# Kernel optimization log

Measured on AMD Instinct MI355X. Metric: run time of the kernel, lower is better.

The kernel has to match this reference:

```python
import jax, jax.numpy as jnp
from jax import lax
import numpy as np

VOCAB, EMBED, HIDDEN, BATCH, MAXLEN = 32000, 512, 1024, 64, 64


def setup_inputs() -> dict:
    key = jax.random.key(0)
    ks = jax.random.split(key, 18)
    s = 0.02
    H, E, V = HIDDEN, EMBED, VOCAB
    return {
        "thought": jax.random.normal(ks[0], (BATCH, H), jnp.float32),
        "emb_table": jax.random.normal(ks[1], (V, E), jnp.float32) * s,
        "w_ih0": jax.random.normal(ks[2], (4 * H, E + H), jnp.float32) * s,
        "w_hh0": jax.random.normal(ks[3], (4 * H, H), jnp.float32) * s,
        "b_ih0": jax.random.normal(ks[4], (4 * H,), jnp.float32) * s,
        "b_hh0": jax.random.normal(ks[5], (4 * H,), jnp.float32) * s,
        "w_ih1": jax.random.normal(ks[6], (4 * H, H), jnp.float32) * s,
        "w_hh1": jax.random.normal(ks[7], (4 * H, H), jnp.float32) * s,
        "b_ih1": jax.random.normal(ks[8], (4 * H,), jnp.float32) * s,
        "b_hh1": jax.random.normal(ks[9], (4 * H,), jnp.float32) * s,
        "gw1": jax.random.normal(ks[10], (H, H), jnp.float32) * s,
        "gb1": jax.random.normal(ks[11], (H,), jnp.float32) * s,
        "gw2": jax.random.normal(ks[12], (1, H), jnp.float32) * s,
        "gb2": jax.random.normal(ks[13], (1,), jnp.float32) * s,
        "out_w": jax.random.normal(ks[14], (V, H), jnp.float32) * s,
        "out_b": jax.random.normal(ks[15], (V,), jnp.float32) * s,
        "max_len": MAXLEN,
    }


def lstm_cell(x, h, c, w_ih, w_hh, b_ih, b_hh):
    # torch nn.LSTM gate order: i, f, g, o
    g = x @ w_ih.T + b_ih + h @ w_hh.T + b_hh
    i, f, gg, o = jnp.split(g, 4, axis=-1)
    c2 = jax.nn.sigmoid(f) * c + jax.nn.sigmoid(i) * jnp.tanh(gg)
    return jax.nn.sigmoid(o) * jnp.tanh(c2), c2


def reference(thought, emb_table, w_ih0, w_hh0, b_ih0, b_hh0, w_ih1, w_hh1,
              b_ih1, b_hh1, gw1, gb1, gw2, gb2, out_w, out_b, max_len):
    """Generation branch of BioDecoder.forward (captions=None), eval mode, epoch=0."""
    B, H = thought.shape
    V = out_w.shape[0]
    temperature, top_p, top_k = 0.9, 0.88, 60
    key = jax.random.key(42)
    rows = jnp.arange(B)[:, None]

    def filt(logits):
        # top-k filter
        kth = lax.top_k(logits, top_k)[0][:, -1:]
        logits = jnp.where(logits < kth, -jnp.inf, logits)
        # nucleus (top-p) filter
        sl, si = lax.top_k(logits, V)  # full descending sort
        cum = jnp.cumsum(jax.nn.softmax(sl, axis=-1), axis=-1)
        rm = cum > top_p
        rm = jnp.concatenate([jnp.zeros_like(rm[:, :1]), rm[:, :-1]], axis=-1)  # always keep best
        mask = jnp.zeros_like(rm).at[rows, si].set(rm)
        return jnp.where(mask, -jnp.inf, logits)

    def step(carry, t):
        h1, c1, h2, c2, prev_ctx, word, counts, hist = carry
        x = jnp.concatenate([emb_table[word], prev_ctx], axis=-1)  # [B, E+H]
        h1, c1 = lstm_cell(x, h1, c1, w_ih0, w_hh0, b_ih0, b_hh0)
        h2, c2 = lstm_cell(h1, h2, c2, w_ih1, w_hh1, b_ih1, b_hh1)
        gate = jax.nn.sigmoid(jnp.tanh(h2 @ gw1.T + gb1) @ gw2.T + gb2)  # [B,1]
        out = h2 * gate
        logits = out @ out_w.T + out_b  # [B, V]
        # recency-decayed repetition penalty over full generated history
        ar = jnp.arange(hist.shape[0])
        w = jnp.where(ar < t, 2.5 * jnp.power(0.8, jnp.maximum(t - ar, 0).astype(jnp.float32)), 0.0)
        pen = jnp.zeros((B, V), logits.dtype).at[rows, hist.T].add(
            jnp.broadcast_to(w[None, :], (B, hist.shape[0])))
        # global count penalty (token_counts shared across batch, as in source)
        logits = logits - pen - jnp.where(counts > 1, 2.0 * counts, 0.0)[None, :]
        logits = logits / temperature + (0.3 / (counts + 1.0))[None, :]
        logits = filt(logits)
        nxt = jax.random.categorical(jax.random.fold_in(key, t), logits, axis=-1)  # [B]
        counts = counts.at[nxt].add(1.0)
        hist = hist.at[t].set(nxt)
        return (h1, c1, h2, c2, out, nxt, counts, hist), nxt

    zeros_h = jnp.zeros_like(thought)
    carry0 = (thought, zeros_h, thought, zeros_h, thought,
              jnp.full((B,), 1, jnp.int32),
              jnp.zeros((V,), jnp.float32),
              jnp.zeros((max_len, B), jnp.int32))
    _, tokens = lax.scan(step, carry0, jnp.arange(max_len))
    return tokens.T  # [B, max_len]
```

## Files before the change

### kernel.cpp

```cpp
#include <hip/hip_runtime.h>
#include <stdint.h>
#include <math.h>

#pragma clang fp contract(off)

#define BATCH 64
#define HID   1024
#define EMBD  512
#define VOC   32000
#define MAXT  64
#define NTOPK 60
#define CAND_MAX 256

__device__ __forceinline__ float xla_tanh(float x) {
  float ax = fabsf(x);
  float xc = fminf(fmaxf(x, -9.0f), 9.0f);
  float x2 = xc * xc;
  float num = -2.76076847742355e-16f;
  num = fmaf(x2, num, 2.00018790482477e-13f);
  num = fmaf(x2, num, -8.60467152213735e-11f);
  num = fmaf(x2, num, 5.12229709037114e-08f);
  num = fmaf(x2, num, 1.48572235717979e-05f);
  num = fmaf(x2, num, 6.37261928875436e-04f);
  num = fmaf(x2, num, 4.89352455891786e-03f);
  num = xc * num;
  float den = 1.19825839466702e-06f;
  den = fmaf(x2, den, 1.18534705686654e-04f);
  den = fmaf(x2, den, 2.26843463243900e-03f);
  den = fmaf(x2, den, 4.89352518554385e-03f);
  float r = num / den;
  return (ax < 0.0004f) ? x : r;
}

__device__ __forceinline__ float xla_sigmoid(float x) {
  return 0.5f * xla_tanh(0.5f * x) + 0.5f;
}

__device__ __forceinline__ float cephes_expf(float _x) {
  float x = fminf(_x, 88.723164f);
  x = fmaxf(x, -88.723164f);
  float m = floorf(fmaf(x, 1.44269504088896341f, 0.5f));
  float r = fmaf(m, -0.693359375f, x);
  r = fmaf(m, 2.12194440e-4f, r);
  float r2 = r * r;
  float r3 = r2 * r;
  float y, y1, y2;
  y  = fmaf(1.9875691500E-4f, r, 1.3981999507E-3f);
  y1 = fmaf(4.1665795894E-2f, r, 1.6666665459E-1f);
  y2 = r + 1.0f;
  y  = fmaf(y, r, 8.3334519073E-3f);
  y1 = fmaf(y1, r, 5.0000001201E-1f);
  y  = fmaf(y, r3, y1);
  y  = fmaf(y, r2, y2);
  float res = ldexpf(y, (int)m);
  return fmaxf(res, _x);
}

__device__ __forceinline__ float cephes_logf(float _x) {
  float x = fmaxf(_x, 1.17549435e-38f);
  unsigned ux = __float_as_uint(x);
  int e_int = (int)(ux >> 23) - 126;
  x = __uint_as_float((ux & 0x007FFFFFu) | 0x3F000000u);
  float e = (float)e_int;
  if (x < 0.707106781186547524f) { e -= 1.0f; x = x + x - 1.0f; }
  else { x = x - 1.0f; }
  float z = x * x;
  float y = 7.0376836292E-2f;
  y = fmaf(y, x, -1.1514610310E-1f);
  y = fmaf(y, x,  1.1676998740E-1f);
  y = fmaf(y, x, -1.2420140846E-1f);
  y = fmaf(y, x,  1.4249322787E-1f);
  y = fmaf(y, x, -1.6668057665E-1f);
  y = fmaf(y, x,  2.0000714765E-1f);
  y = fmaf(y, x, -2.4999993993E-1f);
  y = fmaf(y, x,  3.3333331174E-1f);
  y = y * x;
  y = y * z;
  y = fmaf(e, -2.12194440e-4f, y);
  y = fmaf(-0.5f, z, y);
  float r = x + y;
  r = fmaf(e, 0.693359375f, r);
  return r;
}

__device__ __forceinline__ unsigned rotl32(unsigned v, int s) {
  return (v << s) | (v >> (32 - s));
}
__device__ __forceinline__ void threefry(unsigned k0, unsigned k1,
                                         unsigned& x0, unsigned& x1) {
  unsigned k2 = k0 ^ k1 ^ 0x1BD11BDAu;
  x0 += k0; x1 += k1;
  x0 += x1; x1 = rotl32(x1, 13); x1 ^= x0;
  x0 += x1; x1 = rotl32(x1, 15); x1 ^= x0;
  x0 += x1; x1 = rotl32(x1, 26); x1 ^= x0;
  x0 += x1; x1 = rotl32(x1,  6); x1 ^= x0;
  x0 += k1; x1 += k2 + 1u;
  x0 += x1; x1 = rotl32(x1, 17); x1 ^= x0;
  x0 += x1; x1 = rotl32(x1, 29); x1 ^= x0;
  x0 += x1; x1 = rotl32(x1, 16); x1 ^= x0;
  x0 += x1; x1 = rotl32(x1, 24); x1 ^= x0;
  x0 += k2; x1 += k0 + 2u;
  x0 += x1; x1 = rotl32(x1, 13); x1 ^= x0;
  x0 += x1; x1 = rotl32(x1, 15); x1 ^= x0;
  x0 += x1; x1 = rotl32(x1, 26); x1 ^= x0;
  x0 += x1; x1 = rotl32(x1,  6); x1 ^= x0;
  x0 += k0; x1 += k1 + 3u;
  x0 += x1; x1 = rotl32(x1, 17); x1 ^= x0;
  x0 += x1; x1 = rotl32(x1, 29); x1 ^= x0;
  x0 += x1; x1 = rotl32(x1, 16); x1 ^= x0;
  x0 += x1; x1 = rotl32(x1, 24); x1 ^= x0;
  x0 += k1; x1 += k2 + 4u;
  x0 += x1; x1 = rotl32(x1, 13); x1 ^= x0;
  x0 += x1; x1 = rotl32(x1, 15); x1 ^= x0;
  x0 += x1; x1 = rotl32(x1, 26); x1 ^= x0;
  x0 += x1; x1 = rotl32(x1,  6); x1 ^= x0;
  x0 += k2; x1 += k0 + 5u;
}

__device__ __forceinline__ float gumbel_val(unsigned k0, unsigned k1, int b, int v) {
  unsigned x0 = 0u, x1 = (unsigned)(b * VOC + v);
  threefry(k0, k1, x0, x1);
  unsigned bits = x0 ^ x1;
  float u = __uint_as_float(0x3f800000u | (bits >> 9)) - 1.0f;
  if (u == 0.0f) u = 1.17549435e-38f;
  return -cephes_logf(-cephes_logf(u));
}

__device__ __forceinline__ unsigned okey(float f) {
  unsigned u = __float_as_uint(f);
  return (u & 0x80000000u) ? ~u : (u | 0x80000000u);
}
__device__ __forceinline__ float okey_inv(unsigned key) {
  unsigned u = (key & 0x80000000u) ? (key & 0x7FFFFFFFu) : ~key;
  return __uint_as_float(u);
}

__global__ __launch_bounds__(256) void k_init(const float* __restrict__ thought,
    float* h1a, float* h2a, float* c1, float* c2, float* prev_ctx,
    float* counts, int* word, int* hist) {
  int i = blockIdx.x * blockDim.x + threadIdx.x;
  if (i < BATCH * HID) {
    float tv = thought[i];
    h1a[i] = tv; h2a[i] = tv; prev_ctx[i] = tv;
    c1[i] = 0.f; c2[i] = 0.f;
  }
  if (i < VOC) counts[i] = 0.f;
  if (i < BATCH) word[i] = 1;
  if (i < MAXT * BATCH) hist[i] = 0;
}

__global__ __launch_bounds__(256) void k_gates0f(const float* __restrict__ emb,
    const int* __restrict__ word, const float* __restrict__ prev_ctx,
    const float* __restrict__ h1r, const float* __restrict__ w_ih,
    const float* __restrict__ b_ih, const float* __restrict__ w_hh,
    const float* __restrict__ b_hh, float* __restrict__ h1w,
    float* __restrict__ c1) {
  int jl = threadIdx.x & 7, bg = threadIdx.x >> 3;
  int gate = jl & 3, usel = jl >> 2;
  int u = blockIdx.x * 2 + usel;
  int j = gate * 1024 + u;
  __shared__ float sg[2][4][64];
  const float4* wi4 = (const float4*)(w_ih + (size_t)j * (EMBD + HID));
  const float4* wh4 = (const float4*)(w_hh + (size_t)j * HID);
  const float4* e4[2]; const float4* p4[2]; const float4* h4[2];
  #pragma unroll
  for (int i = 0; i < 2; ++i) {
    int b = bg + 32 * i;
    e4[i] = (const float4*)(emb + (size_t)word[b] * EMBD);
    p4[i] = (const float4*)(prev_ctx + (size_t)b * HID);
    h4[i] = (const float4*)(h1r + (size_t)b * HID);
  }
  float acc[2] = {0.f, 0.f};
  float shh[2] = {0.f, 0.f};
  for (int k = 0; k < EMBD / 4; ++k) {
    float4 w = wi4[k];
    #pragma unroll
    for (int i = 0; i < 2; ++i) {
      float4 a = e4[i][k];
      acc[i] = fmaf(a.x, w.x, acc[i]); acc[i] = fmaf(a.y, w.y, acc[i]);
      acc[i] = fmaf(a.z, w.z, acc[i]); acc[i] = fmaf(a.w, w.w, acc[i]);
    }
  }
  for (int k = 0; k < HID / 4; ++k) {
    float4 w = wi4[EMBD / 4 + k];
    #pragma unroll
    for (int i = 0; i < 2; ++i) {
      float4 a = p4[i][k];
      acc[i] = fmaf(a.x, w.x, acc[i]); acc[i] = fmaf(a.y, w.y, acc[i]);
      acc[i] = fmaf(a.z, w.z, acc[i]); acc[i] = fmaf(a.w, w.w, acc[i]);
    }
  }
  for (int k = 0; k < HID / 4; ++k) {
    float4 w = wh4[k];
    #pragma unroll
    for (int i = 0; i < 2; ++i) {
      float4 a = h4[i][k];
      shh[i] = fmaf(a.x, w.x, shh[i]); shh[i] = fmaf(a.y, w.y, shh[i]);
      shh[i] = fmaf(a.z, w.z, shh[i]); shh[i] = fmaf(a.w, w.w, shh[i]);
    }
  }
  float bi = b_ih[j], bh = b_hh[j];
  #pragma unroll
  for (int i = 0; i < 2; ++i) {
    int b = bg + 32 * i;
    sg[usel][gate][b] = ((acc[i] + bi) + shh[i]) + bh;
  }
  __syncthreads();
  if (threadIdx.x < 128) {
    int us = threadIdx.x >> 6, b = threadIdx.x & 63;
    int uu = blockIdx.x * 2 + us;
    float iv = sg[us][0][b], fv = sg[us][1][b], gv = sg[us][2][b], ov = sg[us][3][b];
    size_t idx = (size_t)b * HID + uu;
    float cold = c1[idx];
    float cnew = xla_sigmoid(fv) * cold + xla_sigmoid(iv) * xla_tanh(gv);
    c1[idx] = cnew;
    h1w[idx] = xla_sigmoid(ov) * xla_tanh(cnew);
  }
}

__global__ __launch_bounds__(256) void k_gates1f(const float* __restrict__ xin,
    const float* __restrict__ hin, const float* __restrict__ w_ih,
    const float* __restrict__ b_ih, const float* __restrict__ w_hh,
    const float* __restrict__ b_hh, float* __restrict__ h2w,
    float* __restrict__ c2) {
  int jl = threadIdx.x & 7, bg = threadIdx.x >> 3;
  int gate = jl & 3, usel = jl >> 2;
  int u = blockIdx.x * 2 + usel;
  int j = gate * 1024 + u;
  __shared__ float sg[2][4][64];
  const float4* wi4 = (const float4*)(w_ih + (size_t)j * HID);
  const float4* wh4 = (const float4*)(w_hh + (size_t)j * HID);
  float acc[2] = {0.f, 0.f};
  float shh[2] = {0.f, 0.f};
  for (int k = 0; k < HID / 4; ++k) {
    float4 w = wi4[k];
    #pragma unroll
    for (int i = 0; i < 2; ++i) {
      float4 a = ((const float4*)(xin + (size_t)(bg + 32 * i) * HID))[k];
      acc[i] = fmaf(a.x, w.x, acc[i]); acc[i] = fmaf(a.y, w.y, acc[i]);
      acc[i] = fmaf(a.z, w.z, acc[i]); acc[i] = fmaf(a.w, w.w, acc[i]);
    }
  }
  for (int k = 0; k < HID / 4; ++k) {
    float4 w = wh4[k];
    #pragma unroll
    for (int i = 0; i < 2; ++i) {
      float4 a = ((const float4*)(hin + (size_t)(bg + 32 * i) * HID))[k];
      shh[i] = fmaf(a.x, w.x, shh[i]); shh[i] = fmaf(a.y, w.y, shh[i]);
      shh[i] = fmaf(a.z, w.z, shh[i]); shh[i] = fmaf(a.w, w.w, shh[i]);
    }
  }
  float bi = b_ih[j], bh = b_hh[j];
  #pragma unroll
  for (int i = 0; i < 2; ++i) {
    int b = bg + 32 * i;
    sg[usel][gate][b] = ((acc[i] + bi) + shh[i]) + bh;
  }
  __syncthreads();
  if (threadIdx.x < 128) {
    int us = threadIdx.x >> 6, b = threadIdx.x & 63;
    int uu = blockIdx.x * 2 + us;
    float iv = sg[us][0][b], fv = sg[us][1][b], gv = sg[us][2][b], ov = sg[us][3][b];
    size_t idx = (size_t)b * HID + uu;
    float cold = c2[idx];
    float cnew = xla_sigmoid(fv) * cold + xla_sigmoid(iv) * xla_tanh(gv);
    c2[idx] = cnew;
    h2w[idx] = xla_sigmoid(ov) * xla_tanh(cnew);
  }
}

__global__ __launch_bounds__(256) void k_gtmp(const float* __restrict__ h2,
    const float* __restrict__ gw1, const float* __restrict__ gb1,
    float* __restrict__ gtmp) {
  int ul = threadIdx.x & 3, b = threadIdx.x >> 2;
  int u = blockIdx.x * 4 + ul;
  const float4* w4 = (const float4*)(gw1 + (size_t)u * HID);
  const float4* a4 = (const float4*)(h2 + (size_t)b * HID);
  float acc = 0.f;
  for (int k = 0; k < HID / 4; ++k) {
    float4 w = w4[k];
    float4 a = a4[k];
    acc = fmaf(a.x, w.x, acc); acc = fmaf(a.y, w.y, acc);
    acc = fmaf(a.z, w.z, acc); acc = fmaf(a.w, w.w, acc);
  }
  gtmp[(size_t)b * HID + u] = xla_tanh(acc + gb1[u]);
}

__global__ __launch_bounds__(256) void k_gateout(const float* __restrict__ gtmp,
    const float* __restrict__ gw2, const float* __restrict__ gb2,
    const float* __restrict__ h2, float* __restrict__ prev_ctx) {
  int b = blockIdx.x, tid = threadIdx.x;
  __shared__ float red[256];
  __shared__ float gsh;
  float s = 0.f;
  for (int k = tid; k < HID; k += 256)
    s = fmaf(gtmp[(size_t)b * HID + k], gw2[k], s);
  red[tid] = s;
  __syncthreads();
  for (int st = 128; st > 0; st >>= 1) {
    if (tid < st) red[tid] += red[tid + st];
    __syncthreads();
  }
  if (tid == 0) gsh = xla_sigmoid(red[0] + gb2[0]);
  __syncthreads();
  float gate = gsh;
  for (int k = tid; k < HID; k += 256)
    prev_ctx[(size_t)b * HID + k] = h2[(size_t)b * HID + k] * gate;
}

__global__ __launch_bounds__(256) void k_logits(const float* __restrict__ outp,
    const float* __restrict__ out_w, const float* __restrict__ out_b,
    const float* __restrict__ counts, float* __restrict__ raw,
    float* __restrict__ adj) {
  int vl = threadIdx.x & 63;
  int v = blockIdx.x * 64 + vl;
  int bbase = __builtin_amdgcn_readfirstlane((int)(threadIdx.x >> 6) * 16);
  const float4* w4 = (const float4*)(out_w + (size_t)v * HID);
  const float4* ob4 = (const float4*)(outp + (size_t)bbase * HID);
  float acc[16];
  #pragma unroll
  for (int i = 0; i < 16; ++i) acc[i] = 0.f;
  for (int k = 0; k < HID / 4; ++k) {
    float4 w = w4[k];
    #pragma unroll
    for (int i = 0; i < 16; ++i) {
      float4 a = ob4[k + 256 * i];
      acc[i] = fmaf(a.x, w.x, acc[i]); acc[i] = fmaf(a.y, w.y, acc[i]);
      acc[i] = fmaf(a.z, w.z, acc[i]); acc[i] = fmaf(a.w, w.w, acc[i]);
    }
  }
  float c = counts[v];
  float cpen = (c > 1.0f) ? (2.0f * c) : 0.0f;
  float bonus = 0.3f / (c + 1.0f);
  float bv = out_b[v];
  #pragma unroll
  for (int i = 0; i < 16; ++i) {
    int b = bbase + i;
    float r = acc[i] + bv;
    raw[(size_t)b * VOC + v] = r;
    adj[(size_t)b * VOC + v] = (r - cpen) / 0.9f + bonus;
  }
}

__global__ __launch_bounds__(256) void k_sample(float* __restrict__ adj,
    const float* __restrict__ raw, float* __restrict__ counts,
    int* __restrict__ word, int* __restrict__ hist,
    int* __restrict__ out_tokens, int t) {
  int b = blockIdx.x, tid = threadIdx.x;
  float* row = adj + (size_t)b * VOC;
  __shared__ unsigned keys[VOC];
  __shared__ int wcnt[4];
  __shared__ int sh_cnt;
  __shared__ float cval[CAND_MAX];
  __shared__ int cidx[CAND_MAX];
  __shared__ float sval[CAND_MAX];
  __shared__ int sidx[CAND_MAX];
  __shared__ unsigned char kept[CAND_MAX];
  __shared__ float rval[256];
  __shared__ int ridx[256];
  __shared__ unsigned shk0, shk1;
  __shared__ int hcol[MAXT];
  __shared__ float wtab[MAXT];

  if (tid < t) hcol[tid] = hist[tid * BATCH + b];
  if (tid < MAXT) wtab[tid] = 2.5f * powf(0.8f, (float)tid);
  if (tid == 0) {
    sh_cnt = 0;
    unsigned a = 0u, cc = (unsigned)t;
    threefry(0u, 42u, a, cc);
    shk0 = a; shk1 = cc;
  }
  __syncthreads();

  if (tid < t) {
    int ar = tid;
    int tok = hcol[ar];
    bool first = true;
    for (int a2 = 0; a2 < ar; ++a2)
      if (hcol[a2] == tok) { first = false; break; }
    if (first) {
      float pen = 0.f;
      for (int a2 = ar; a2 < t; ++a2)
        if (hcol[a2] == tok) pen += wtab[t - a2];
      float c = counts[tok];
      float cpen = (c > 1.0f) ? (2.0f * c) : 0.0f;
      float bonus = 0.3f / (c + 1.0f);
      float r = raw[(size_t)b * VOC + tok];
      row[tok] = ((r - pen) - cpen) / 0.9f + bonus;
    }
  }
  __syncthreads();

  const float4* row4 = (const float4*)row;
  uint4* keys4 = (uint4*)keys;
  for (int i = tid; i < VOC / 4; i += 256) {
    float4 f = row4[i];
    uint4 kk;
    kk.x = okey(f.x); kk.y = okey(f.y); kk.z = okey(f.z); kk.w = okey(f.w);
    keys4[i] = kk;
  }
  __syncthreads();

  unsigned long long lo = 0ULL, hi = 1ULL << 32;
  for (int it = 0; it < 32; ++it) {
    unsigned mid = (unsigned)((lo + hi) >> 1);
    int cnt = 0;
    for (int i = tid; i < VOC / 4; i += 256) {
      uint4 kk = keys4[i];
      cnt += (kk.x >= mid) ? 1 : 0;
      cnt += (kk.y >= mid) ? 1 : 0;
      cnt += (kk.z >= mid) ? 1 : 0;
      cnt += (kk.w >= mid) ? 1 : 0;
    }
    #pragma unroll
    for (int off = 32; off > 0; off >>= 1)
      cnt += __shfl_xor(cnt, off, 64);
    if ((tid & 63) == 0) wcnt[tid >> 6] = cnt;
    __syncthreads();
    int total = wcnt[0] + wcnt[1] + wcnt[2] + wcnt[3];
    if (total >= NTOPK) lo = (unsigned long long)mid;
    else                hi = (unsigned long long)mid;
    __syncthreads();
  }
  unsigned kmin = (unsigned)lo;

  for (int v = tid; v < VOC; v += 256) {
    unsigned key = keys[v];
    if (key >= kmin) {
      int pos = atomicAdd(&sh_cnt, 1);
      if (pos < CAND_MAX) { cval[pos] = okey_inv(key); cidx[pos] = v; }
    }
  }
  __syncthreads();
  int C = sh_cnt; if (C > CAND_MAX) C = CAND_MAX;

  for (int i = tid; i < C; i += 256) {
    float vi = cval[i]; int ii = cidx[i]; int r = 0;
    for (int j = 0; j < C; ++j) {
      float vj = cval[j]; int ij = cidx[j];
      if (vj > vi || (vj == vi && ij < ii)) ++r;
    }
    sval[r] = vi; sidx[r] = ii;
  }
  __syncthreads();

  if (tid == 0) {
    float m = sval[0];
    float psum = 0.f;
    for (int j = 0; j < C; ++j) {
      float p = cephes_expf(sval[j] - m);
      cval[j] = p;
      psum += p;
    }
    float cum = 0.f;
    for (int j = 0; j < C; ++j) {
      kept[j] = (j == 0 || cum <= 0.88f) ? 1 : 0;
      cum += cval[j] / psum;
    }
  }
  __syncthreads();

  float bscore = -INFINITY; int bidx = 0x7FFFFFFF;
  for (int j = tid; j < C; j += 256) {
    if (kept[j]) {
      float gv = gumbel_val(shk0, shk1, b, sidx[j]);
      float sc = gv + sval[j];
      if (sc > bscore || (sc == bscore && sidx[j] < bidx)) { bscore = sc; bidx = sidx[j]; }
    }
  }
  rval[tid] = bscore; ridx[tid] = bidx;
  __syncthreads();
  for (int s = 128; s > 0; s >>= 1) {
    if (tid < s) {
      float ov = rval[tid + s]; int oi = ridx[tid + s];
      if (ov > rval[tid] || (ov == rval[tid] && oi < ridx[tid])) {
        rval[tid] = ov; ridx[tid] = oi;
      }
    }
    __syncthreads();
  }
  if (tid == 0) {
    int tok = ridx[0];
    word[b] = tok;
    hist[t * BATCH + b] = tok;
    out_tokens[b * MAXT + t] = tok;
    atomicAdd(&counts[tok], 1.0f);
  }
}

extern "C" void kernel_launch(void* const* d_in, const int* in_sizes, int n_in,
                              void* d_out, int out_size, void* d_ws, size_t ws_size,
                              hipStream_t stream) {
  const float* thought = (const float*)d_in[0];
  const float* emb     = (const float*)d_in[1];
  const float* w_ih0   = (const float*)d_in[2];
  const float* w_hh0   = (const float*)d_in[3];
  const float* b_ih0   = (const float*)d_in[4];
  const float* b_hh0   = (const float*)d_in[5];
  const float* w_ih1   = (const float*)d_in[6];
  const float* w_hh1   = (const float*)d_in[7];
  const float* b_ih1   = (const float*)d_in[8];
  const float* b_hh1   = (const float*)d_in[9];
  const float* gw1     = (const float*)d_in[10];
  const float* gb1     = (const float*)d_in[11];
  const float* gw2     = (const float*)d_in[12];
  const float* gb2     = (const float*)d_in[13];
  const float* out_w   = (const float*)d_in[14];
  const float* out_b   = (const float*)d_in[15];
  int* out_tokens = (int*)d_out;

  float* F = (float*)d_ws;
  float* h1a      = F;
  float* h1b      = F + 65536;
  float* h2a      = F + 131072;
  float* h2b      = F + 196608;
  float* c1       = F + 262144;
  float* c2       = F + 327680;
  float* prev_ctx = F + 393216;
  float* gtmp     = F + 458752;
  float* counts   = F + 524288;
  float* raw      = F + 556288;
  float* adj      = F + 2604288;
  int*   word     = (int*)(F + 4652288);
  int*   hist     = word + 64;

  k_init<<<256, 256, 0, stream>>>(thought, h1a, h2a, c1, c2, prev_ctx, counts, word, hist);
  for (int t = 0; t < MAXT; ++t) {
    const float* h1r = (t & 1) ? h1b : h1a;
    float*       h1w = (t & 1) ? h1a : h1b;
    const float* h2r = (t & 1) ? h2b : h2a;
    float*       h2w = (t & 1) ? h2a : h2b;
    k_gates0f<<<512, 256, 0, stream>>>(emb, word, prev_ctx, h1r, w_ih0, b_ih0, w_hh0, b_hh0, h1w, c1);
    k_gates1f<<<512, 256, 0, stream>>>(h1w, h2r, w_ih1, b_ih1, w_hh1, b_hh1, h2w, c2);
    k_gtmp<<<256, 256, 0, stream>>>(h2w, gw1, gb1, gtmp);
    k_gateout<<<64, 256, 0, stream>>>(gtmp, gw2, gb2, h2w, prev_ctx);
    k_logits<<<500, 256, 0, stream>>>(prev_ctx, out_w, out_b, counts, raw, adj);
    k_sample<<<64, 256, 0, stream>>>(adj, raw, counts, word, hist, out_tokens, t);
  }
}
```

Before: 39.32 ms.

## Fuse per-step LSTM decode kernels into one persistent kernel with grid barriers

Replaces the six kernel launches per time step (LSTM layer 0, layer 1, gate MLP, gate output, logits, sampling) and the init kernel with one persistent kernel of 224 blocks. The phases are separated by a software grid barrier built on an atomic counter. This removes hundreds of launches and their gaps, and drops the gtmp scratch buffer. Each block now handles four hidden units per LSTM iteration instead of two. The cost is that the large shared-memory key array limits each CU to one resident block, so occupancy in the memory-bound matvecs drops. The kernel also relies on all 224 blocks being co-resident, otherwise the spinning barrier deadlocks.

```diff
diff --git a/kernel.cpp b/kernel.cpp
--- a/kernel.cpp
+++ b/kernel.cpp
@@ -11,6 +11,7 @@
 #define MAXT  64
 #define NTOPK 60
 #define CAND_MAX 256
+#define NB    224
 
 __device__ __forceinline__ float xla_tanh(float x) {
   float ax = fabsf(x);
@@ -135,221 +136,35 @@
   return __uint_as_float(u);
 }
 
-__global__ __launch_bounds__(256) void k_init(const float* __restrict__ thought,
-    float* h1a, float* h2a, float* c1, float* c2, float* prev_ctx,
-    float* counts, int* word, int* hist) {
-  int i = blockIdx.x * blockDim.x + threadIdx.x;
-  if (i < BATCH * HID) {
-    float tv = thought[i];
-    h1a[i] = tv; h2a[i] = tv; prev_ctx[i] = tv;
-    c1[i] = 0.f; c2[i] = 0.f;
-  }
-  if (i < VOC) counts[i] = 0.f;
-  if (i < BATCH) word[i] = 1;
-  if (i < MAXT * BATCH) hist[i] = 0;
-}
-
-__global__ __launch_bounds__(256) void k_gates0f(const float* __restrict__ emb,
-    const int* __restrict__ word, const float* __restrict__ prev_ctx,
-    const float* __restrict__ h1r, const float* __restrict__ w_ih,
-    const float* __restrict__ b_ih, const float* __restrict__ w_hh,
-    const float* __restrict__ b_hh, float* __restrict__ h1w,
-    float* __restrict__ c1) {
-  int jl = threadIdx.x & 7, bg = threadIdx.x >> 3;
-  int gate = jl & 3, usel = jl >> 2;
-  int u = blockIdx.x * 2 + usel;
-  int j = gate * 1024 + u;
-  __shared__ float sg[2][4][64];
-  const float4* wi4 = (const float4*)(w_ih + (size_t)j * (EMBD + HID));
-  const float4* wh4 = (const float4*)(w_hh + (size_t)j * HID);
-  const float4* e4[2]; const float4* p4[2]; const float4* h4[2];
-  #pragma unroll
-  for (int i = 0; i < 2; ++i) {
-    int b = bg + 32 * i;
-    e4[i] = (const float4*)(emb + (size_t)word[b] * EMBD);
-    p4[i] = (const float4*)(prev_ctx + (size_t)b * HID);
-    h4[i] = (const float4*)(h1r + (size_t)b * HID);
-  }
-  float acc[2] = {0.f, 0.f};
-  float shh[2] = {0.f, 0.f};
-  for (int k = 0; k < EMBD / 4; ++k) {
-    float4 w = wi4[k];
-    #pragma unroll
-    for (int i = 0; i < 2; ++i) {
-      float4 a = e4[i][k];
-      acc[i] = fmaf(a.x, w.x, acc[i]); acc[i] = fmaf(a.y, w.y, acc[i]);
-      acc[i] = fmaf(a.z, w.z, acc[i]); acc[i] = fmaf(a.w, w.w, acc[i]);
-    }
-  }
-  for (int k = 0; k < HID / 4; ++k) {
-    float4 w = wi4[EMBD / 4 + k];
-    #pragma unroll
-    for (int i = 0; i < 2; ++i) {
-      float4 a = p4[i][k];
-      acc[i] = fmaf(a.x, w.x, acc[i]); acc[i] = fmaf(a.y, w.y, acc[i]);
-      acc[i] = fmaf(a.z, w.z, acc[i]); acc[i] = fmaf(a.w, w.w, acc[i]);
-    }
-  }
-  for (int k = 0; k < HID / 4; ++k) {
-    float4 w = wh4[k];
-    #pragma unroll
-    for (int i = 0; i < 2; ++i) {
-      float4 a = h4[i][k];
-      shh[i] = fmaf(a.x, w.x, shh[i]); shh[i] = fmaf(a.y, w.y, shh[i]);
-      shh[i] = fmaf(a.z, w.z, shh[i]); shh[i] = fmaf(a.w, w.w, shh[i]);
-    }
-  }
-  float bi = b_ih[j], bh = b_hh[j];
-  #pragma unroll
-  for (int i = 0; i < 2; ++i) {
-    int b = bg + 32 * i;
-    sg[usel][gate][b] = ((acc[i] + bi) + shh[i]) + bh;
+__device__ __forceinline__ void gbar(unsigned* cnt, unsigned target) {
+  __syncthreads();
+  if (threadIdx.x == 0) {
+    __threadfence();
+    __hip_atomic_fetch_add(cnt, 1u, __ATOMIC_RELAXED, __HIP_MEMORY_SCOPE_AGENT);
+    while (__hip_atomic_load(cnt, __ATOMIC_RELAXED, __HIP_MEMORY_SCOPE_AGENT) < target)
+      __builtin_amdgcn_s_sleep(16);
+    __threadfence();
   }
   __syncthreads();
-  if (threadIdx.x < 128) {
-    int us = threadIdx.x >> 6, b = threadIdx.x & 63;
-    int uu = blockIdx.x * 2 + us;
-    float iv = sg[us][0][b], fv = sg[us][1][b], gv = sg[us][2][b], ov = sg[us][3][b];
-    size_t idx = (size_t)b * HID + uu;
-    float cold = c1[idx];
-    float cnew = xla_sigmoid(fv) * cold + xla_sigmoid(iv) * xla_tanh(gv);
-    c1[idx] = cnew;
-    h1w[idx] = xla_sigmoid(ov) * xla_tanh(cnew);
-  }
-}
-
-__global__ __launch_bounds__(256) void k_gates1f(const float* __restrict__ xin,
-    const float* __restrict__ hin, const float* __restrict__ w_ih,
-    const float* __restrict__ b_ih, const float* __restrict__ w_hh,
-    const float* __restrict__ b_hh, float* __restrict__ h2w,
-    float* __restrict__ c2) {
-  int jl = threadIdx.x & 7, bg = threadIdx.x >> 3;
-  int gate = jl & 3, usel = jl >> 2;
-  int u = blockIdx.x * 2 + usel;
-  int j = gate * 1024 + u;
-  __shared__ float sg[2][4][64];
-  const float4* wi4 = (const float4*)(w_ih + (size_t)j * HID);
-  const float4* wh4 = (const float4*)(w_hh + (size_t)j * HID);
-  float acc[2] = {0.f, 0.f};
-  float shh[2] = {0.f, 0.f};
-  for (int k = 0; k < HID / 4; ++k) {
-    float4 w = wi4[k];
-    #pragma unroll
-    for (int i = 0; i < 2; ++i) {
-      float4 a = ((const float4*)(xin + (size_t)(bg + 32 * i) * HID))[k];
-      acc[i] = fmaf(a.x, w.x, acc[i]); acc[i] = fmaf(a.y, w.y, acc[i]);
-      acc[i] = fmaf(a.z, w.z, acc[i]); acc[i] = fmaf(a.w, w.w, acc[i]);
-    }
-  }
-  for (int k = 0; k < HID / 4; ++k) {
-    float4 w = wh4[k];
-    #pragma unroll
-    for (int i = 0; i < 2; ++i) {
-      float4 a = ((const float4*)(hin + (size_t)(bg + 32 * i) * HID))[k];
-      shh[i] = fmaf(a.x, w.x, shh[i]); shh[i] = fmaf(a.y, w.y, shh[i]);
-      shh[i] = fmaf(a.z, w.z, shh[i]); shh[i] = fmaf(a.w, w.w, shh[i]);
-    }
-  }
-  float bi = b_ih[j], bh = b_hh[j];
-  #pragma unroll
-  for (int i = 0; i < 2; ++i) {
-    int b = bg + 32 * i;
-    sg[usel][gate][b] = ((acc[i] + bi) + shh[i]) + bh;
-  }
-  __syncthreads();
-  if (threadIdx.x < 128) {
-    int us = threadIdx.x >> 6, b = threadIdx.x & 63;
-    int uu = blockIdx.x * 2 + us;
-    float iv = sg[us][0][b], fv = sg[us][1][b], gv = sg[us][2][b], ov = sg[us][3][b];
-    size_t idx = (size_t)b * HID + uu;
-    float cold = c2[idx];
-    float cnew = xla_sigmoid(fv) * cold + xla_sigmoid(iv) * xla_tanh(gv);
-    c2[idx] = cnew;
-    h2w[idx] = xla_sigmoid(ov) * xla_tanh(cnew);
-  }
-}
-
-__global__ __launch_bounds__(256) void k_gtmp(const float* __restrict__ h2,
+}
+
+__global__ __launch_bounds__(256) void k_mega(
+    const float* __restrict__ thought, const float* __restrict__ emb,
+    const float* __restrict__ w_ih0, const float* __restrict__ b_ih0,
+    const float* __restrict__ w_hh0, const float* __restrict__ b_hh0,
+    const float* __restrict__ w_ih1, const float* __restrict__ b_ih1,
+    const float* __restrict__ w_hh1, const float* __restrict__ b_hh1,
     const float* __restrict__ gw1, const float* __restrict__ gb1,
-    float* __restrict__ gtmp) {
-  int ul = threadIdx.x & 3, b = threadIdx.x >> 2;
-  int u = blockIdx.x * 4 + ul;
-  const float4* w4 = (const float4*)(gw1 + (size_t)u * HID);
-  const float4* a4 = (const float4*)(h2 + (size_t)b * HID);
-  float acc = 0.f;
-  for (int k = 0; k < HID / 4; ++k) {
-    float4 w = w4[k];
-    float4 a = a4[k];
-    acc = fmaf(a.x, w.x, acc); acc = fmaf(a.y, w.y, acc);
-    acc = fmaf(a.z, w.z, acc); acc = fmaf(a.w, w.w, acc);
-  }
-  gtmp[(size_t)b * HID + u] = xla_tanh(acc + gb1[u]);
-}
-
-__global__ __launch_bounds__(256) void k_gateout(const float* __restrict__ gtmp,
     const float* __restrict__ gw2, const float* __restrict__ gb2,
-    const float* __restrict__ h2, float* __restrict__ prev_ctx) {
-  int b = blockIdx.x, tid = threadIdx.x;
+    const float* __restrict__ out_w, const float* __restrict__ out_b,
+    float* h1a, float* h1b, float* h2a, float* h2b, float* c1, float* c2,
+    float* prev_ctx, float* counts, float* raw, float* adj,
+    int* word, int* hist, int* out_tokens, unsigned* bar) {
+
+  __shared__ __align__(16) unsigned keys[VOC];
   __shared__ float red[256];
-  __shared__ float gsh;
-  float s = 0.f;
-  for (int k = tid; k < HID; k += 256)
-    s = fmaf(gtmp[(size_t)b * HID + k], gw2[k], s);
-  red[tid] = s;
-  __syncthreads();
-  for (int st = 128; st > 0; st >>= 1) {
-    if (tid < st) red[tid] += red[tid + st];
-    __syncthreads();
-  }
-  if (tid == 0) gsh = xla_sigmoid(red[0] + gb2[0]);
-  __syncthreads();
-  float gate = gsh;
-  for (int k = tid; k < HID; k += 256)
-    prev_ctx[(size_t)b * HID + k] = h2[(size_t)b * HID + k] * gate;
-}
-
-__global__ __launch_bounds__(256) void k_logits(const float* __restrict__ outp,
-    const float* __restrict__ out_w, const float* __restrict__ out_b,
-    const float* __restrict__ counts, float* __restrict__ raw,
-    float* __restrict__ adj) {
-  int vl = threadIdx.x & 63;
-  int v = blockIdx.x * 64 + vl;
-  int bbase = __builtin_amdgcn_readfirstlane((int)(threadIdx.x >> 6) * 16);
-  const float4* w4 = (const float4*)(out_w + (size_t)v * HID);
-  const float4* ob4 = (const float4*)(outp + (size_t)bbase * HID);
-  float acc[16];
-  #pragma unroll
-  for (int i = 0; i < 16; ++i) acc[i] = 0.f;
-  for (int k = 0; k < HID / 4; ++k) {
-    float4 w = w4[k];
-    #pragma unroll
-    for (int i = 0; i < 16; ++i) {
-      float4 a = ob4[k + 256 * i];
-      acc[i] = fmaf(a.x, w.x, acc[i]); acc[i] = fmaf(a.y, w.y, acc[i]);
-      acc[i] = fmaf(a.z, w.z, acc[i]); acc[i] = fmaf(a.w, w.w, acc[i]);
-    }
-  }
-  float c = counts[v];
-  float cpen = (c > 1.0f) ? (2.0f * c) : 0.0f;
-  float bonus = 0.3f / (c + 1.0f);
-  float bv = out_b[v];
-  #pragma unroll
-  for (int i = 0; i < 16; ++i) {
-    int b = bbase + i;
-    float r = acc[i] + bv;
-    raw[(size_t)b * VOC + v] = r;
-    adj[(size_t)b * VOC + v] = (r - cpen) / 0.9f + bonus;
-  }
-}
-
-__global__ __launch_bounds__(256) void k_sample(float* __restrict__ adj,
-    const float* __restrict__ raw, float* __restrict__ counts,
-    int* __restrict__ word, int* __restrict__ hist,
-    int* __restrict__ out_tokens, int t) {
-  int b = blockIdx.x, tid = threadIdx.x;
-  float* row = adj + (size_t)b * VOC;
-  __shared__ unsigned keys[VOC];
-  __shared__ int wcnt[4];
+  __shared__ float gshv;
+  __shared__ int wcnt4[4];
   __shared__ int sh_cnt;
   __shared__ float cval[CAND_MAX];
   __shared__ int cidx[CAND_MAX];
@@ -362,129 +177,345 @@
   __shared__ int hcol[MAXT];
   __shared__ float wtab[MAXT];
 
-  if (tid < t) hcol[tid] = hist[tid * BATCH + b];
-  if (tid < MAXT) wtab[tid] = 2.5f * powf(0.8f, (float)tid);
-  if (tid == 0) {
-    sh_cnt = 0;
-    unsigned a = 0u, cc = (unsigned)t;
-    threefry(0u, 42u, a, cc);
-    shk0 = a; shk1 = cc;
+  float (*sg)[4][64] = (float (*)[4][64])keys;
+  float* gt = (float*)keys;
+
+  const int blk = blockIdx.x, tid = threadIdx.x;
+  unsigned bt = 0;
+
+  for (int i = blk * 256 + tid; i < BATCH * HID; i += NB * 256) {
+    float tv = thought[i];
+    h1a[i] = tv; h2a[i] = tv; prev_ctx[i] = tv;
+    c1[i] = 0.f; c2[i] = 0.f;
   }
-  __syncthreads();
-
-  if (tid < t) {
-    int ar = tid;
-    int tok = hcol[ar];
-    bool first = true;
-    for (int a2 = 0; a2 < ar; ++a2)
-      if (hcol[a2] == tok) { first = false; break; }
-    if (first) {
-      float pen = 0.f;
-      for (int a2 = ar; a2 < t; ++a2)
-        if (hcol[a2] == tok) pen += wtab[t - a2];
-      float c = counts[tok];
-      float cpen = (c > 1.0f) ? (2.0f * c) : 0.0f;
-      float bonus = 0.3f / (c + 1.0f);
-      float r = raw[(size_t)b * VOC + tok];
-      row[tok] = ((r - pen) - cpen) / 0.9f + bonus;
+  for (int i = blk * 256 + tid; i < VOC; i += NB * 256) counts[i] = 0.f;
+  for (int i = blk * 256 + tid; i < MAXT * BATCH; i += NB * 256) hist[i] = 0;
+  for (int i = blk * 256 + tid; i < BATCH; i += NB * 256) word[i] = 1;
+  gbar(bar, (++bt) * NB);
+
+  for (int t = 0; t < MAXT; ++t) {
+    const float* h1r = (t & 1) ? h1b : h1a;
+    float*       h1w = (t & 1) ? h1a : h1b;
+    const float* h2r = (t & 1) ? h2b : h2a;
+    float*       h2w = (t & 1) ? h2a : h2b;
+
+    {
+      int jl = tid & 15, bg = tid >> 4;
+      int gate = jl & 3, usel = jl >> 2;
+      for (int uq = blk; uq < 256; uq += NB) {
+        int u = uq * 4 + usel;
+        int j = gate * 1024 + u;
+        const float4* wi4 = (const float4*)(w_ih0 + (size_t)j * (EMBD + HID));
+        const float4* wh4 = (const float4*)(w_hh0 + (size_t)j * HID);
+        const float4* e4[4]; const float4* p4[4]; const float4* h4[4];
+        #pragma unroll
+        for (int i = 0; i < 4; ++i) {
+          int b = bg + 16 * i;
+          e4[i] = (const float4*)(emb + (size_t)word[b] * EMBD);
+          p4[i] = (const float4*)(prev_ctx + (size_t)b * HID);
+          h4[i] = (const float4*)(h1r + (size_t)b * HID);
+        }
+        float acc[4] = {0.f, 0.f, 0.f, 0.f};
+        float shh[4] = {0.f, 0.f, 0.f, 0.f};
+        for (int k = 0; k < EMBD / 4; ++k) {
+          float4 w = wi4[k];
+          #pragma unroll
+          for (int i = 0; i < 4; ++i) {
+            float4 a = e4[i][k];
+            acc[i] = fmaf(a.x, w.x, acc[i]); acc[i] = fmaf(a.y, w.y, acc[i]);
+            acc[i] = fmaf(a.z, w.z, acc[i]); acc[i] = fmaf(a.w, w.w, acc[i]);
+          }
+        }
+        for (int k = 0; k < HID / 4; ++k) {
+          float4 w = wi4[EMBD / 4 + k];
+          #pragma unroll
+          for (int i = 0; i < 4; ++i) {
+            float4 a = p4[i][k];
+            acc[i] = fmaf(a.x, w.x, acc[i]); acc[i] = fmaf(a.y, w.y, acc[i]);
+            acc[i] = fmaf(a.z, w.z, acc[i]); acc[i] = fmaf(a.w, w.w, acc[i]);
+          }
+        }
+        for (int k = 0; k < HID / 4; ++k) {
+          float4 w = wh4[k];
+          #pragma unroll
+          for (int i = 0; i < 4; ++i) {
+            float4 a = h4[i][k];
+            shh[i] = fmaf(a.x, w.x, shh[i]); shh[i] = fmaf(a.y, w.y, shh[i]);
+            shh[i] = fmaf(a.z, w.z, shh[i]); shh[i] = fmaf(a.w, w.w, shh[i]);
+          }
+        }
+        float bi = b_ih0[j], bh = b_hh0[j];
+        #pragma unroll
+        for (int i = 0; i < 4; ++i) {
+          int b = bg + 16 * i;
+          sg[usel][gate][b] = ((acc[i] + bi) + shh[i]) + bh;
+        }
+        __syncthreads();
+        {
+          int us = tid >> 6, b = tid & 63;
+          int uu = uq * 4 + us;
+          float iv = sg[us][0][b], fv = sg[us][1][b], gv = sg[us][2][b], ov = sg[us][3][b];
+          size_t idx = (size_t)b * HID + uu;
+          float cold = c1[idx];
+          float cnew = xla_sigmoid(fv) * cold + xla_sigmoid(iv) * xla_tanh(gv);
+          c1[idx] = cnew;
+          h1w[idx] = xla_sigmoid(ov) * xla_tanh(cnew);
+        }
+        __syncthreads();
+      }
     }
-  }
-  __syncthreads();
-
-  const float4* row4 = (const float4*)row;
-  uint4* keys4 = (uint4*)keys;
-  for (int i = tid; i < VOC / 4; i += 256) {
-    float4 f = row4[i];
-    uint4 kk;
-    kk.x = okey(f.x); kk.y = okey(f.y); kk.z = okey(f.z); kk.w = okey(f.w);
-    keys4[i] = kk;
-  }
-  __syncthreads();
-
-  unsigned long long lo = 0ULL, hi = 1ULL << 32;
-  for (int it = 0; it < 32; ++it) {
-    unsigned mid = (unsigned)((lo + hi) >> 1);
-    int cnt = 0;
-    for (int i = tid; i < VOC / 4; i += 256) {
-      uint4 kk = keys4[i];
-      cnt += (kk.x >= mid) ? 1 : 0;
-      cnt += (kk.y >= mid) ? 1 : 0;
-      cnt += (kk.z >= mid) ? 1 : 0;
-      cnt += (kk.w >= mid) ? 1 : 0;
+    gbar(bar, (++bt) * NB);
+
+    {
+      int jl = tid & 15, bg = tid >> 4;
+      int gate = jl & 3, usel = jl >> 2;
+      for (int uq = blk; uq < 256; uq += NB) {
+        int u = uq * 4 + usel;
+        int j = gate * 1024 + u;
+        const float4* wi4 = (const float4*)(w_ih1 + (size_t)j * HID);
+        const float4* wh4 = (const float4*)(w_hh1 + (size_t)j * HID);
+        float acc[4] = {0.f, 0.f, 0.f, 0.f};
+        float shh[4] = {0.f, 0.f, 0.f, 0.f};
+        for (int k = 0; k < HID / 4; ++k) {
+          float4 w = wi4[k];
+          #pragma unroll
+          for (int i = 0; i < 4; ++i) {
+            float4 a = ((const float4*)(h1w + (size_t)(bg + 16 * i) * HID))[k];
+            acc[i] = fmaf(a.x, w.x, acc[i]); acc[i] = fmaf(a.y, w.y, acc[i]);
+            acc[i] = fmaf(a.z, w.z, acc[i]); acc[i] = fmaf(a.w, w.w, acc[i]);
+          }
+        }
+        for (int k = 0; k < HID / 4; ++k) {
+          float4 w = wh4[k];
+          #pragma unroll
+          for (int i = 0; i < 4; ++i) {
+            float4 a = ((const float4*)(h2r + (size_t)(bg + 16 * i) * HID))[k];
+            shh[i] = fmaf(a.x, w.x, shh[i]); shh[i] = fmaf(a.y, w.y, shh[i]);
+            shh[i] = fmaf(a.z, w.z, shh[i]); shh[i] = fmaf(a.w, w.w, shh[i]);
+          }
+        }
+        float bi = b_ih1[j], bh = b_hh1[j];
+        #pragma unroll
+        for (int i = 0; i < 4; ++i) {
+          int b = bg + 16 * i;
+          sg[usel][gate][b] = ((acc[i] + bi) + shh[i]) + bh;
+        }
+        __syncthreads();
+        {
+          int us = tid >> 6, b = tid & 63;
+          int uu = uq * 4 + us;
+          float iv = sg[us][0][b], fv = sg[us][1][b], gv = sg[us][2][b], ov = sg[us][3][b];
+          size_t idx = (size_t)b * HID + uu;
+          float cold = c2[idx];
+          float cnew = xla_sigmoid(fv) * cold + xla_sigmoid(iv) * xla_tanh(gv);
+          c2[idx] = cnew;
+          h2w[idx] = xla_sigmoid(ov) * xla_tanh(cnew);
+        }
+        __syncthreads();
+      }
     }
-    #pragma unroll
-    for (int off = 32; off > 0; off >>= 1)
-      cnt += __shfl_xor(cnt, off, 64);
-    if ((tid & 63) == 0) wcnt[tid >> 6] = cnt;
-    __syncthreads();
-    int total = wcnt[0] + wcnt[1] + wcnt[2] + wcnt[3];
-    if (total >= NTOPK) lo = (unsigned long long)mid;
-    else                hi = (unsigned long long)mid;
-    __syncthreads();
-  }
-  unsigned kmin = (unsigned)lo;
-
-  for (int v = tid; v < VOC; v += 256) {
-    unsigned key = keys[v];
-    if (key >= kmin) {
-      int pos = atomicAdd(&sh_cnt, 1);
-      if (pos < CAND_MAX) { cval[pos] = okey_inv(key); cidx[pos] = v; }
+    gbar(bar, (++bt) * NB);
+
+    if (blk < BATCH) {
+      int b = blk;
+      const float4* a4 = (const float4*)(h2w + (size_t)b * HID);
+      for (int r = 0; r < 4; ++r) {
+        int u = tid + 256 * r;
+        const float4* w4 = (const float4*)(gw1 + (size_t)u * HID);
+        float acc = 0.f;
+        for (int k = 0; k < HID / 4; ++k) {
+          float4 w = w4[k];
+          float4 a = a4[k];
+          acc = fmaf(a.x, w.x, acc); acc = fmaf(a.y, w.y, acc);
+          acc = fmaf(a.z, w.z, acc); acc = fmaf(a.w, w.w, acc);
+        }
+        gt[u] = xla_tanh(acc + gb1[u]);
+      }
+      __syncthreads();
+      float s = 0.f;
+      for (int k = tid; k < HID; k += 256)
+        s = fmaf(gt[k], gw2[k], s);
+      red[tid] = s;
+      __syncthreads();
+      for (int st = 128; st > 0; st >>= 1) {
+        if (tid < st) red[tid] += red[tid + st];
+        __syncthreads();
+      }
+      if (tid == 0) gshv = xla_sigmoid(red[0] + gb2[0]);
+      __syncthreads();
+      float gate = gshv;
+      for (int k = tid; k < HID; k += 256)
+        prev_ctx[(size_t)b * HID + k] = h2w[(size_t)b * HID + k] * gate;
     }
-  }
-  __syncthreads();
-  int C = sh_cnt; if (C > CAND_MAX) C = CAND_MAX;
-
-  for (int i = tid; i < C; i += 256) {
-    float vi = cval[i]; int ii = cidx[i]; int r = 0;
-    for (int j = 0; j < C; ++j) {
-      float vj = cval[j]; int ij = cidx[j];
-      if (vj > vi || (vj == vi && ij < ii)) ++r;
+    gbar(bar, (++bt) * NB);
+
+    {
+      int lz;
+      asm volatile("v_mov_b32 %0, 0" : "=v"(lz));
+      int vl = tid & 63;
+      int bbase = (tid >> 6) * 16;
+      const float4* ap = (const float4*)(prev_ctx + (size_t)bbase * HID + lz);
+      for (int ch = blk; ch < 500; ch += NB) {
+        int v = ch * 64 + vl;
+        const float4* w4 = (const float4*)(out_w + (size_t)v * HID);
+        float acc[16];
+        #pragma unroll
+        for (int i = 0; i < 16; ++i) acc[i] = 0.f;
+        for (int k = 0; k < HID / 4; ++k) {
+          float4 w = w4[k];
+          #pragma unroll
+          for (int i = 0; i < 16; ++i) {
+            float4 a = ap[k + 256 * i];
+            acc[i] = fmaf(a.x, w.x, acc[i]); acc[i] = fmaf(a.y, w.y, acc[i]);
+            acc[i] = fmaf(a.z, w.z, acc[i]); acc[i] = fmaf(a.w, w.w, acc[i]);
+          }
+        }
+        float c = counts[v];
+        float cpen = (c > 1.0f) ? (2.0f * c) : 0.0f;
+        float bonus = 0.3f / (c + 1.0f);
+        float bv = out_b[v];
+        #pragma unroll
+        for (int i = 0; i < 16; ++i) {
+          int b = bbase + i;
+          float r = acc[i] + bv;
+          raw[(size_t)b * VOC + v] = r;
+          adj[(size_t)b * VOC + v] = (r - cpen) / 0.9f + bonus;
+        }
+      }
     }
-    sval[r] = vi; sidx[r] = ii;
-  }
-  __syncthreads();
-
-  if (tid == 0) {
-    float m = sval[0];
-    float psum = 0.f;
-    for (int j = 0; j < C; ++j) {
-      float p = cephes_expf(sval[j] - m);
-      cval[j] = p;
-      psum += p;
+    gbar(bar, (++bt) * NB);
+
+    if (blk < BATCH) {
+      int b = blk;
+      float* row = adj + (size_t)b * VOC;
+
+      if (tid < t) hcol[tid] = hist[tid * BATCH + b];
+      if (tid < MAXT) wtab[tid] = 2.5f * powf(0.8f, (float)tid);
+      if (tid == 0) {
+        sh_cnt = 0;
+        unsigned a = 0u, cc = (unsigned)t;
+        threefry(0u, 42u, a, cc);
+        shk0 = a; shk1 = cc;
+      }
+      __syncthreads();
+
+      if (tid < t) {
+        int ar = tid;
+        int tok = hcol[ar];
+        bool first = true;
+        for (int a2 = 0; a2 < ar; ++a2)
+          if (hcol[a2] == tok) { first = false; break; }
+        if (first) {
+          float pen = 0.f;
+          for (int a2 = ar; a2 < t; ++a2)
+            if (hcol[a2] == tok) pen += wtab[t - a2];
+          float c = counts[tok];
+          float cpen = (c > 1.0f) ? (2.0f * c) : 0.0f;
+          float bonus = 0.3f / (c + 1.0f);
+          float r = raw[(size_t)b * VOC + tok];
+          row[tok] = ((r - pen) - cpen) / 0.9f + bonus;
+        }
+      }
+      __syncthreads();
+
+      const float4* row4 = (const float4*)row;
+      uint4* keys4 = (uint4*)keys;
+      for (int i = tid; i < VOC / 4; i += 256) {
+        float4 f = row4[i];
+        uint4 kk;
+        kk.x = okey(f.x); kk.y = okey(f.y); kk.z = okey(f.z); kk.w = okey(f.w);
+        keys4[i] = kk;
+      }
+      __syncthreads();
+
+      unsigned long long lo = 0ULL, hi = 1ULL << 32;
+      for (int it = 0; it < 32; ++it) {
+        unsigned mid = (unsigned)((lo + hi) >> 1);
+        int cnt = 0;
+        for (int i = tid; i < VOC / 4; i += 256) {
+          uint4 kk = keys4[i];
+          cnt += (kk.x >= mid) ? 1 : 0;
+          cnt += (kk.y >= mid) ? 1 : 0;
+          cnt += (kk.z >= mid) ? 1 : 0;
+          cnt += (kk.w >= mid) ? 1 : 0;
+        }
+        #pragma unroll
+        for (int off = 32; off > 0; off >>= 1)
+          cnt += __shfl_xor(cnt, off, 64);
+        if ((tid & 63) == 0) wcnt4[tid >> 6] = cnt;
+        __syncthreads();
+        int total = wcnt4[0] + wcnt4[1] + wcnt4[2] + wcnt4[3];
+        if (total >= NTOPK) lo = (unsigned long long)mid;
+        else                hi = (unsigned long long)mid;
+        __syncthreads();
+      }
+      unsigned kmin = (unsigned)lo;
+
+      for (int v = tid; v < VOC; v += 256) {
+        unsigned key = keys[v];
+        if (key >= kmin) {
+          int pos = atomicAdd(&sh_cnt, 1);
+          if (pos < CAND_MAX) { cval[pos] = okey_inv(key); cidx[pos] = v; }
+        }
+      }
+      __syncthreads();
+      int C = sh_cnt; if (C > CAND_MAX) C = CAND_MAX;
+
+      for (int i = tid; i < C; i += 256) {
+        float vi = cval[i]; int ii = cidx[i]; int r = 0;
+        for (int j = 0; j < C; ++j) {
+          float vj = cval[j]; int ij = cidx[j];
+          if (vj > vi || (vj == vi && ij < ii)) ++r;
+        }
+        sval[r] = vi; sidx[r] = ii;
+      }
+      __syncthreads();
+
+      if (tid == 0) {
+        float m = sval[0];
+        float psum = 0.f;
+        for (int j = 0; j < C; ++j) {
+          float p = cephes_expf(sval[j] - m);
+          cval[j] = p;
+          psum += p;
+        }
+        float cum = 0.f;
+        for (int j = 0; j < C; ++j) {
+          kept[j] = (j == 0 || cum <= 0.88f) ? 1 : 0;
+          cum += cval[j] / psum;
+        }
+      }
+      __syncthreads();
+
+      float bscore = -INFINITY; int bidx = 0x7FFFFFFF;
+      for (int j = tid; j < C; j += 256) {
+        if (kept[j]) {
+          float gv = gumbel_val(shk0, shk1, b, sidx[j]);
+          float sc = gv + sval[j];
+          if (sc > bscore || (sc == bscore && sidx[j] < bidx)) { bscore = sc; bidx = sidx[j]; }
+        }
+      }
+      rval[tid] = bscore; ridx[tid] = bidx;
+      __syncthreads();
+      for (int s = 128; s > 0; s >>= 1) {
+        if (tid < s) {
+          float ov = rval[tid + s]; int oi = ridx[tid + s];
+          if (ov > rval[tid] || (ov == rval[tid] && oi < ridx[tid])) {
+            rval[tid] = ov; ridx[tid] = oi;
+          }
+        }
+        __syncthreads();
+      }
+      if (tid == 0) {
+        int tok = ridx[0];
+        word[b] = tok;
+        hist[t * BATCH + b] = tok;
+        out_tokens[b * MAXT + t] = tok;
+        atomicAdd(&counts[tok], 1.0f);
+      }
+      __syncthreads();
     }
-    float cum = 0.f;
-    for (int j = 0; j < C; ++j) {
-      kept[j] = (j == 0 || cum <= 0.88f) ? 1 : 0;
-      cum += cval[j] / psum;
-    }
-  }
-  __syncthreads();
-
-  float bscore = -INFINITY; int bidx = 0x7FFFFFFF;
-  for (int j = tid; j < C; j += 256) {
-    if (kept[j]) {
-      float gv = gumbel_val(shk0, shk1, b, sidx[j]);
-      float sc = gv + sval[j];
-      if (sc > bscore || (sc == bscore && sidx[j] < bidx)) { bscore = sc; bidx = sidx[j]; }
-    }
-  }
-  rval[tid] = bscore; ridx[tid] = bidx;
-  __syncthreads();
-  for (int s = 128; s > 0; s >>= 1) {
-    if (tid < s) {
-      float ov = rval[tid + s]; int oi = ridx[tid + s];
-      if (ov > rval[tid] || (ov == rval[tid] && oi < ridx[tid])) {
-        rval[tid] = ov; ridx[tid] = oi;
-      }
-    }
-    __syncthreads();
-  }
-  if (tid == 0) {
-    int tok = ridx[0];
-    word[b] = tok;
-    hist[t * BATCH + b] = tok;
-    out_tokens[b * MAXT + t] = tok;
-    atomicAdd(&counts[tok], 1.0f);
+    gbar(bar, (++bt) * NB);
   }
 }
 
@@ -517,24 +548,17 @@
   float* c1       = F + 262144;
   float* c2       = F + 327680;
   float* prev_ctx = F + 393216;
-  float* gtmp     = F + 458752;
-  float* counts   = F + 524288;
-  float* raw      = F + 556288;
-  float* adj      = F + 2604288;
-  int*   word     = (int*)(F + 4652288);
+  float* counts   = F + 458752;
+  float* raw      = F + 490752;
+  float* adj      = F + 2538752;
+  int*   word     = (int*)(F + 4586752);
   int*   hist     = word + 64;
-
-  k_init<<<256, 256, 0, stream>>>(thought, h1a, h2a, c1, c2, prev_ctx, counts, word, hist);
-  for (int t = 0; t < MAXT; ++t) {
-    const float* h1r = (t & 1) ? h1b : h1a;
-    float*       h1w = (t & 1) ? h1a : h1b;
-    const float* h2r = (t & 1) ? h2b : h2a;
-    float*       h2w = (t & 1) ? h2a : h2b;
-    k_gates0f<<<512, 256, 0, stream>>>(emb, word, prev_ctx, h1r, w_ih0, b_ih0, w_hh0, b_hh0, h1w, c1);
-    k_gates1f<<<512, 256, 0, stream>>>(h1w, h2r, w_ih1, b_ih1, w_hh1, b_hh1, h2w, c2);
-    k_gtmp<<<256, 256, 0, stream>>>(h2w, gw1, gb1, gtmp);
-    k_gateout<<<64, 256, 0, stream>>>(gtmp, gw2, gb2, h2w, prev_ctx);
-    k_logits<<<500, 256, 0, stream>>>(prev_ctx, out_w, out_b, counts, raw, adj);
-    k_sample<<<64, 256, 0, stream>>>(adj, raw, counts, word, hist, out_tokens, t);
-  }
-}
+  unsigned* bar   = (unsigned*)(F + 4590912);
+
+  hipMemsetAsync(bar, 0, 64, stream);
+  k_mega<<<NB, 256, 0, stream>>>(thought, emb,
+      w_ih0, b_ih0, w_hh0, b_hh0, w_ih1, b_ih1, w_hh1, b_hh1,
+      gw1, gb1, gw2, gb2, out_w, out_b,
+      h1a, h1b, h2a, h2b, c1, c2, prev_ctx, counts, raw, adj,
+      word, hist, out_tokens, bar);
+}
```

Result: slower. 102.6 ms (+161.0%).
